# Performance work log

Hardware: AMD Instinct MI355X
Metric: run time of the kernel (lower is better)

The kernel has to match this reference:

```python
import jax, jax.numpy as jnp
import numpy as np

TAU = 1.0
K_TAU = 1.0
MAX_K = 64


def setup_inputs() -> dict:
    key = jax.random.key(0)
    ks = jax.random.split(key, 6)
    B, S, D, H = 8, 4096, 1024, 2048
    token_embeddings = jax.random.normal(ks[0], (B, S, D), dtype=jnp.float32)
    W1 = jax.random.normal(ks[1], (D, H), dtype=jnp.float32) * (1.0 / np.sqrt(D))
    b1 = jnp.zeros((H,), dtype=jnp.float32)
    W2 = jax.random.normal(ks[2], (H, 1), dtype=jnp.float32) * (1.0 / np.sqrt(H))
    b2 = jnp.zeros((1,), dtype=jnp.float32)
    k_logits = jax.random.normal(ks[3], (MAX_K,), dtype=jnp.float32) * 0.02
    return {"token_embeddings": token_embeddings, "W1": W1, "b1": b1,
            "W2": W2, "b2": b2, "k_logits": k_logits}


def _gumbel(rng, shape):
    u = jax.random.uniform(rng, shape, minval=1e-08, maxval=1.0 - 1e-08)
    return -jnp.log(-jnp.log(u))


def reference(token_embeddings, W1, b1, W2, b2, k_logits):
    B, S, D = token_embeddings.shape
    # scorer: Dense -> relu -> Dense(1), squeeze -> [B, S]
    h = jax.nn.relu(jnp.einsum('bsd,dh->bsh', token_embeddings, W1) + b1)
    importance_logits = (jnp.einsum('bsh,ho->bso', h, W2) + b2)[..., 0]

    rng = jax.random.key(42)  # training rng
    rng1, rng2 = jax.random.split(rng)

    # learnable-k selection (training branch)
    k_gumbel = _gumbel(rng1, k_logits.shape)
    k_soft = jax.nn.softmax((k_logits + k_gumbel) / K_TAU)
    expected_k = jnp.sum(k_soft * jnp.arange(1, MAX_K + 1, dtype=k_soft.dtype))
    k_selected = jnp.argmax(k_soft) + 1  # traced int scalar

    # gumbel-softmax hard top-k over tokens
    perturbed = importance_logits + _gumbel(rng2, importance_logits.shape)
    soft_mask = jax.nn.softmax(perturbed / TAU, axis=-1)  # [B, S]
    # rank of each token (0 = smallest); top-k == rank >= S - k
    rank = jnp.argsort(jnp.argsort(soft_mask, axis=-1), axis=-1)
    hard_mask = (rank >= S - k_selected).astype(soft_mask.dtype)
    selection_mask = jax.lax.stop_gradient(hard_mask - soft_mask) + soft_mask

    filtered_embeddings = token_embeddings * selection_mask[..., None]
    return filtered_embeddings, selection_mask, expected_k
```

## Files before the change

### kernel.cpp

```cpp
#include <hip/hip_runtime.h>
#include <stdint.h>

#define B_BATCH 8
#define S_SEQ   4096
#define D_DIM   1024
#define H_DIM   2048
#define M_TOK   (B_BATCH * S_SEQ)
#define MAXK    64
#define NSPLIT  2

typedef unsigned int u32;
typedef unsigned short u16;
typedef unsigned long long u64;
typedef __attribute__((ext_vector_type(8))) short short8;
typedef __attribute__((ext_vector_type(4))) float f32x4;

#define GLOBAL_AS __attribute__((address_space(1)))
#define LDS_AS    __attribute__((address_space(3)))


#define TF_ROUND(x0, x1, r) { x0 += x1; x1 = ((x1 << r) | (x1 >> (32 - r))); x1 ^= x0; }

__device__ __forceinline__ void tf2x32(u32 k0, u32 k1, u32 x0, u32 x1, u32& o0, u32& o1) {
  u32 k2 = k0 ^ k1 ^ 0x1BD11BDAu;
  x0 += k0; x1 += k1;
  TF_ROUND(x0, x1, 13) TF_ROUND(x0, x1, 15) TF_ROUND(x0, x1, 26) TF_ROUND(x0, x1, 6)
  x0 += k1; x1 += k2 + 1u;
  TF_ROUND(x0, x1, 17) TF_ROUND(x0, x1, 29) TF_ROUND(x0, x1, 16) TF_ROUND(x0, x1, 24)
  x0 += k2; x1 += k0 + 2u;
  TF_ROUND(x0, x1, 13) TF_ROUND(x0, x1, 15) TF_ROUND(x0, x1, 26) TF_ROUND(x0, x1, 6)
  x0 += k0; x1 += k1 + 3u;
  TF_ROUND(x0, x1, 17) TF_ROUND(x0, x1, 29) TF_ROUND(x0, x1, 16) TF_ROUND(x0, x1, 24)
  x0 += k1; x1 += k2 + 4u;
  TF_ROUND(x0, x1, 13) TF_ROUND(x0, x1, 15) TF_ROUND(x0, x1, 26) TF_ROUND(x0, x1, 6)
  x0 += k2; x1 += k0 + 5u;
  o0 = x0; o1 = x1;
}

__device__ __forceinline__ void jax_subkeys(u32& r1a, u32& r1b, u32& r2a, u32& r2b) {
  tf2x32(0u, 42u, 0u, 0u, r1a, r1b);
  tf2x32(0u, 42u, 0u, 1u, r2a, r2b);
}

__device__ __forceinline__ u32 jax_bits32(u32 ka, u32 kb, u32 i) {
  u32 o0, o1;
  tf2x32(ka, kb, 0u, i, o0, o1);
  return o0 ^ o1;
}

__device__ __forceinline__ float jax_uniform_from_bits(u32 bits) {
  float f = __uint_as_float((bits >> 9) | 0x3f800000u) - 1.0f;
  float r = f + 1e-8f;
  return fmaxf(1e-8f, r);
}

__device__ __forceinline__ float gumbel_from_bits(u32 bits) {
  float u = jax_uniform_from_bits(bits);
  return -logf(-logf(u));
}

__device__ __forceinline__ u32 ordf(float v) {
  u32 b = __float_as_uint(v);
  return (b & 0x80000000u) ? ~b : (b | 0x80000000u);
}

__device__ __forceinline__ u64 shflx64(u64 v, int m) {
  unsigned lo = (unsigned)v, hi = (unsigned)(v >> 32);
  lo = (unsigned)__shfl_xor((int)lo, m);
  hi = (unsigned)__shfl_xor((int)hi, m);
  return ((u64)hi << 32) | lo;
}


__device__ __forceinline__ u16 f2bf_rn(float x) {
  u32 u = __float_as_uint(x);
  u32 r = u + 0x7fffu + ((u >> 16) & 1u);
  return (u16)(r >> 16);
}

__device__ __forceinline__ void split1(float x, u16& h, u16& lo) {
  h = f2bf_rn(x);
  float hf = __uint_as_float(((u32)h) << 16);
  lo = f2bf_rn(x - hf);
}


__global__ __launch_bounds__(256) void split_a_kernel(const float* __restrict__ x,
                                                      u16* __restrict__ hi,
                                                      u16* __restrict__ lo) {
  const size_t i = ((size_t)blockIdx.x * 256 + threadIdx.x) * 4;
  float4 v = *(const float4*)(x + i);
  u16 h0, h1, h2, h3, l0, l1, l2, l3;
  split1(v.x, h0, l0); split1(v.y, h1, l1); split1(v.z, h2, l2); split1(v.w, h3, l3);
  u64 hv = (u64)h0 | ((u64)h1 << 16) | ((u64)h2 << 32) | ((u64)h3 << 48);
  u64 lv = (u64)l0 | ((u64)l1 << 16) | ((u64)l2 << 32) | ((u64)l3 << 48);
  *(u64*)(hi + i) = hv;
  *(u64*)(lo + i) = lv;
}

__global__ __launch_bounds__(256) void split_w1t_kernel(const float* __restrict__ W1,
                                                        u16* __restrict__ bhi,
                                                        u16* __restrict__ blo) {
  __shared__ float tile[32][33];
  const int tx = threadIdx.x & 31, ty = threadIdx.x >> 5;
  const int n0 = blockIdx.x * 32, k0 = blockIdx.y * 32;
  #pragma unroll
  for (int r = 0; r < 4; ++r)
    tile[ty + r * 8][tx] = W1[(size_t)(k0 + ty + r * 8) * H_DIM + n0 + tx];
  __syncthreads();
  #pragma unroll
  for (int r = 0; r < 4; ++r) {
    const int n = n0 + ty + r * 8, k = k0 + tx;
    u16 h, l;
    split1(tile[tx][ty + r * 8], h, l);
    bhi[(size_t)n * D_DIM + k] = h;
    blo[(size_t)n * D_DIM + k] = l;
  }
}


__device__ __forceinline__ void stage16(const u16* g, u16* l) {
  __builtin_amdgcn_global_load_lds((const GLOBAL_AS u32*)g, (LDS_AS u32*)l, 16, 0, 0);
}

__global__ __launch_bounds__(256, 2) void scorer_mfma(
    const u16* __restrict__ Ahi, const u16* __restrict__ Alo,
    const u16* __restrict__ Bhi, const u16* __restrict__ Blo,
    const float* __restrict__ b1, const float* __restrict__ W2,
    float* __restrict__ pl) {
  __shared__ u16 smem[4 * 128 * 32];
  u16* sAhi = smem;
  u16* sAlo = smem + 4096;
  u16* sBhi = smem + 8192;
  u16* sBlo = smem + 12288;

  const int tid = threadIdx.x;
  const int w = tid >> 6;
  const int l = tid & 63;
  const int m0 = blockIdx.x * 128;
  const int nyb = blockIdx.y;

  const int rl0 = w * 32 + (l >> 2);
  const int rl1 = rl0 + 16;
  const int kloc0 = (((l & 3) ^ ((rl0 >> 1) & 3)) << 3);
  const int kloc1 = (((l & 3) ^ ((rl1 >> 1) & 3)) << 3);
  const int lb0 = (w * 32) * 32;
  const int lb1 = (w * 32 + 16) * 32;

  int a_off[4], b_off[4];
  #pragma unroll
  for (int i = 0; i < 4; ++i) {
    int row = ((w & 1) << 6) + i * 16 + (l & 15);
    int slot = (l >> 4) ^ ((row >> 1) & 3);
    a_off[i] = row * 32 + slot * 8;
    int nrow = ((w >> 1) << 6) + i * 16 + (l & 15);
    int nslot = (l >> 4) ^ ((nrow >> 1) & 3);
    b_off[i] = nrow * 32 + nslot * 8;
  }

  float logit[4][4];
  #pragma unroll
  for (int i = 0; i < 4; ++i)
    #pragma unroll
    for (int r = 0; r < 4; ++r) logit[i][r] = 0.f;

  for (int t8 = 0; t8 < H_DIM / (128 * NSPLIT); ++t8) {
    const int n0 = nyb * (H_DIM / NSPLIT) + t8 * 128;
    f32x4 acc[4][4];
    #pragma unroll
    for (int i = 0; i < 4; ++i)
      #pragma unroll
      for (int j = 0; j < 4; ++j) acc[i][j] = (f32x4){0.f, 0.f, 0.f, 0.f};

    const u16* pA0h = Ahi + (size_t)(m0 + rl0) * D_DIM + kloc0;
    const u16* pA1h = Ahi + (size_t)(m0 + rl1) * D_DIM + kloc1;
    const u16* pA0l = Alo + (size_t)(m0 + rl0) * D_DIM + kloc0;
    const u16* pA1l = Alo + (size_t)(m0 + rl1) * D_DIM + kloc1;
    const u16* pB0h = Bhi + (size_t)(n0 + rl0) * D_DIM + kloc0;
    const u16* pB1h = Bhi + (size_t)(n0 + rl1) * D_DIM + kloc1;
    const u16* pB0l = Blo + (size_t)(n0 + rl0) * D_DIM + kloc0;
    const u16* pB1l = Blo + (size_t)(n0 + rl1) * D_DIM + kloc1;

    for (int k0 = 0; k0 < D_DIM; k0 += 32) {
      __syncthreads();
      stage16(pA0h, sAhi + lb0); stage16(pA1h, sAhi + lb1);
      stage16(pA0l, sAlo + lb0); stage16(pA1l, sAlo + lb1);
      stage16(pB0h, sBhi + lb0); stage16(pB1h, sBhi + lb1);
      stage16(pB0l, sBlo + lb0); stage16(pB1l, sBlo + lb1);
      pA0h += 32; pA1h += 32; pA0l += 32; pA1l += 32;
      pB0h += 32; pB1h += 32; pB0l += 32; pB1l += 32;
      __syncthreads();

      short8 ah[4], al[4], bh[4], bl[4];
      #pragma unroll
      for (int i = 0; i < 4; ++i) {
        ah[i] = *(const short8*)(sAhi + a_off[i]);
        al[i] = *(const short8*)(sAlo + a_off[i]);
        bh[i] = *(const short8*)(sBhi + b_off[i]);
        bl[i] = *(const short8*)(sBlo + b_off[i]);
      }
      #pragma unroll
      for (int i = 0; i < 4; ++i)
        #pragma unroll
        for (int j = 0; j < 4; ++j) {
          acc[i][j] = __builtin_amdgcn_mfma_f32_16x16x32_bf16(ah[i], bh[j], acc[i][j], 0, 0, 0);
          acc[i][j] = __builtin_amdgcn_mfma_f32_16x16x32_bf16(ah[i], bl[j], acc[i][j], 0, 0, 0);
          acc[i][j] = __builtin_amdgcn_mfma_f32_16x16x32_bf16(al[i], bh[j], acc[i][j], 0, 0, 0);
        }
    }

    const int nb = n0 + ((w >> 1) << 6);
    #pragma unroll
    for (int j = 0; j < 4; ++j) {
      const int n = nb + j * 16 + (l & 15);
      const float b1v = b1[n];
      const float w2v = W2[n];
      #pragma unroll
      for (int i = 0; i < 4; ++i)
        #pragma unroll
        for (int r = 0; r < 4; ++r)
          logit[i][r] += fmaxf(acc[i][j][r] + b1v, 0.f) * w2v;
    }
  }

  __syncthreads();
  float* red = (float*)smem;
  const int col = (l & 15) + ((w >> 1) << 4);
  #pragma unroll
  for (int i = 0; i < 4; ++i)
    #pragma unroll
    for (int r = 0; r < 4; ++r) {
      const int m = ((w & 1) << 6) + i * 16 + ((l >> 4) << 2) + r;
      red[m * 33 + col] = logit[i][r];
    }
  __syncthreads();
  if (tid < 128) {
    float s = 0.f;
    #pragma unroll
    for (int x = 0; x < 32; ++x) s += red[tid * 33 + x];
    pl[(size_t)nyb * M_TOK + m0 + tid] = s;
  }
}


__global__ __launch_bounds__(256) void scorer_kernel(
    const float* __restrict__ emb, const float* __restrict__ W1,
    const float* __restrict__ b1, const float* __restrict__ W2,
    const float* __restrict__ b2, float* __restrict__ pert) {
  __shared__ float As[16][68];
  __shared__ float Bs[16][132];
  __shared__ float red[64][17];

  const int tid = threadIdx.x;
  const int tx = tid & 15;
  const int ty = tid >> 4;
  const int m0 = blockIdx.x * 64;
  const int at = tid >> 2;
  const int ac = (tid & 3) << 2;
  const int br = tid >> 4;
  const int bc = (tid & 15) << 3;

  float logit[4] = {0.f, 0.f, 0.f, 0.f};

  for (int n0 = 0; n0 < H_DIM; n0 += 128) {
    float acc[4][8];
    #pragma unroll
    for (int i = 0; i < 4; i++)
      #pragma unroll
      for (int j = 0; j < 8; j++) acc[i][j] = 0.f;

    for (int k0 = 0; k0 < D_DIM; k0 += 16) {
      float4 av  = *(const float4*)(emb + (size_t)(m0 + at) * D_DIM + (k0 + ac));
      float4 bv0 = *(const float4*)(W1 + (size_t)(k0 + br) * H_DIM + (n0 + bc));
      float4 bv1 = *(const float4*)(W1 + (size_t)(k0 + br) * H_DIM + (n0 + bc) + 4);
      __syncthreads();
      As[ac + 0][at] = av.x; As[ac + 1][at] = av.y;
      As[ac + 2][at] = av.z; As[ac + 3][at] = av.w;
      *(float4*)&Bs[br][bc]     = bv0;
      *(float4*)&Bs[br][bc + 4] = bv1;
      __syncthreads();
      #pragma unroll
      for (int k = 0; k < 16; k++) {
        float4 a   = *(const float4*)&As[k][ty << 2];
        float4 b0  = *(const float4*)&Bs[k][tx << 3];
        float4 b1v = *(const float4*)&Bs[k][(tx << 3) + 4];
        float aa[4] = {a.x, a.y, a.z, a.w};
        float bb[8] = {b0.x, b0.y, b0.z, b0.w, b1v.x, b1v.y, b1v.z, b1v.w};
        #pragma unroll
        for (int i = 0; i < 4; i++)
          #pragma unroll
          for (int j = 0; j < 8; j++)
            acc[i][j] = fmaf(aa[i], bb[j], acc[i][j]);
      }
    }
    float4 c0 = *(const float4*)(b1 + n0 + (tx << 3));
    float4 c1 = *(const float4*)(b1 + n0 + (tx << 3) + 4);
    float4 w0 = *(const float4*)(W2 + n0 + (tx << 3));
    float4 w1 = *(const float4*)(W2 + n0 + (tx << 3) + 4);
    float cb[8] = {c0.x, c0.y, c0.z, c0.w, c1.x, c1.y, c1.z, c1.w};
    float wb[8] = {w0.x, w0.y, w0.z, w0.w, w1.x, w1.y, w1.z, w1.w};
    #pragma unroll
    for (int i = 0; i < 4; i++)
      #pragma unroll
      for (int j = 0; j < 8; j++) {
        float h = fmaxf(acc[i][j] + cb[j], 0.f);
        logit[i] = fmaf(h, wb[j], logit[i]);
      }
  }

  __syncthreads();
  #pragma unroll
  for (int i = 0; i < 4; i++) red[(ty << 2) + i][tx] = logit[i];
  __syncthreads();

  if (tid < 64) {
    float s = 0.f;
    #pragma unroll
    for (int x = 0; x < 16; x++) s += red[tid][x];
    s += b2[0];
    int t = m0 + tid;
    u32 r1a, r1b, r2a, r2b;
    jax_subkeys(r1a, r1b, r2a, r2b);
    pert[t] = s + gumbel_from_bits(jax_bits32(r2a, r2b, (u32)t));
  }
}


template <bool FROM_PL>
__device__ __forceinline__ void topk_body(const float* kl, const float* pl,
                                          const float* b2, float* mask,
                                          float* expk) {
  const int r = blockIdx.x;
  const int tid = threadIdx.x;
  const int w = tid >> 6, l = tid & 63;
  __shared__ int ksel_sh;
  __shared__ int cnt[2][4];

  u32 r1a, r1b, r2a, r2b;
  jax_subkeys(r1a, r1b, r2a, r2b);

  if (tid < 64) {
    float p = kl[l] + gumbel_from_bits(jax_bits32(r1a, r1b, (u32)l));
    u64 kkey = ((u64)ordf(p) << 32) | (unsigned)(63 - l);
    #pragma unroll
    for (int off = 32; off >= 1; off >>= 1) {
      u64 o = shflx64(kkey, off);
      if (o > kkey) kkey = o;
    }
    if (l == 0) ksel_sh = 64 - (int)(kkey & 0xffffffffu);
    if (r == 0) {
      float m = p;
      #pragma unroll
      for (int off = 32; off >= 1; off >>= 1) m = fmaxf(m, __shfl_xor(m, off));
      float e = expf(p - m);
      float s = e;
      #pragma unroll
      for (int off = 32; off >= 1; off >>= 1) s += __shfl_xor(s, off);
      float v = (e / s) * (float)(l + 1);
      #pragma unroll
      for (int off = 32; off >= 1; off >>= 1) v += __shfl_xor(v, off);
      if (l == 0) expk[0] = v;
    }
  }
  __syncthreads();
  const int k = ksel_sh;
  const float b2v = FROM_PL ? b2[0] : 0.f;

  u64 keys[16];
  #pragma unroll
  for (int j = 0; j < 16; j++) {
    int s = tid + (j << 8);
    int t = (r << 12) + s;
    float v;
    if (FROM_PL) {
      float acc = pl[t];
      #pragma unroll
      for (int q = 1; q < NSPLIT; ++q) acc += pl[(size_t)q * M_TOK + t];
      v = acc + b2v + gumbel_from_bits(jax_bits32(r2a, r2b, (u32)t));
    } else {
      v = mask[t];
    }
    keys[j] = ((u64)ordf(v) << 12) | (unsigned)s;
  }

  u64 lo = 0ull, hi = (1ull << 44) - 1ull;
  int it = 0;
  while (lo < hi) {
    const u64 mid = (lo + hi + 1ull) >> 1;
    int c = 0;
    #pragma unroll
    for (int j = 0; j < 16; j++) c += (keys[j] >= mid) ? 1 : 0;
    #pragma unroll
    for (int off = 32; off >= 1; off >>= 1) c += __shfl_xor(c, off);
    const int buf = it & 1;
    if (l == 0) cnt[buf][w] = c;
    __syncthreads();
    const int tot = cnt[buf][0] + cnt[buf][1] + cnt[buf][2] + cnt[buf][3];
    if (tot >= k) lo = mid; else hi = mid - 1ull;
    ++it;
  }
  const u64 thresh = lo;

  #pragma unroll
  for (int j = 0; j < 16; j++) {
    int s = tid + (j << 8);
    mask[(r << 12) + s] = (keys[j] >= thresh) ? 1.0f : 0.0f;
  }
}

__global__ __launch_bounds__(256) void topk_pl_kernel(const float* __restrict__ kl,
                                                      const float* __restrict__ pl,
                                                      const float* __restrict__ b2,
                                                      float* __restrict__ mask,
                                                      float* __restrict__ expk) {
  topk_body<true>(kl, pl, b2, mask, expk);
}

__global__ __launch_bounds__(256) void topk_kernel(const float* __restrict__ kl,
                                                   float* __restrict__ mask,
                                                   float* __restrict__ expk) {
  topk_body<false>(kl, nullptr, nullptr, mask, expk);
}


__global__ __launch_bounds__(256) void filter_kernel(const float* __restrict__ emb,
                                                     const float* __restrict__ mask,
                                                     float* __restrict__ out) {
  const int t = blockIdx.x;
  const float mk = mask[t];
  const size_t base = (size_t)t * D_DIM + ((size_t)threadIdx.x << 2);
  float4 v = *(const float4*)(emb + base);
  *(float4*)(out + base) = make_float4(v.x * mk, v.y * mk, v.z * mk, v.w * mk);
}


extern "C" void kernel_launch(void* const* d_in, const int* in_sizes, int n_in,
                              void* d_out, int out_size, void* d_ws, size_t ws_size,
                              hipStream_t stream) {
  const float* emb = (const float*)d_in[0];
  const float* W1  = (const float*)d_in[1];
  const float* b1  = (const float*)d_in[2];
  const float* W2  = (const float*)d_in[3];
  const float* b2  = (const float*)d_in[4];
  const float* kl  = (const float*)d_in[5];
  float* out  = (float*)d_out;
  float* mask = out + (size_t)M_TOK * D_DIM;
  float* expk = mask + M_TOK;

  const size_t ws_need = (size_t)H_DIM * D_DIM * 2 * 2 + (size_t)NSPLIT * M_TOK * 4;

  if (ws_size >= ws_need) {
    u16* Ahi = (u16*)d_out;
    u16* Alo = Ahi + (size_t)M_TOK * D_DIM;
    u16* Bhi = (u16*)d_ws;
    u16* Blo = Bhi + (size_t)H_DIM * D_DIM;
    float* pl = (float*)(Blo + (size_t)H_DIM * D_DIM);

    split_a_kernel<<<M_TOK * D_DIM / 1024, 256, 0, stream>>>(emb, Ahi, Alo);
    split_w1t_kernel<<<dim3(H_DIM / 32, D_DIM / 32), 256, 0, stream>>>(W1, Bhi, Blo);
    scorer_mfma<<<dim3(M_TOK / 128, NSPLIT), 256, 0, stream>>>(Ahi, Alo, Bhi, Blo, b1, W2, pl);
    topk_pl_kernel<<<B_BATCH, 256, 0, stream>>>(kl, pl, b2, mask, expk);
  } else {
    scorer_kernel<<<M_TOK / 64, 256, 0, stream>>>(emb, W1, b1, W2, b2, mask);
    topk_kernel<<<B_BATCH, 256, 0, stream>>>(kl, mask, expk);
  }

  filter_kernel<<<M_TOK, 256, 0, stream>>>(emb, mask, out);
}
```

Measured before the change: 707.5 us.

## Fuse split kernels, remap scorer blocks across XCDs, grid-stride filter

```diff
diff --git a/kernel.cpp b/kernel.cpp
--- a/kernel.cpp
+++ b/kernel.cpp
@@ -85,36 +85,40 @@
 }
 
 
-__global__ __launch_bounds__(256) void split_a_kernel(const float* __restrict__ x,
-                                                      u16* __restrict__ hi,
-                                                      u16* __restrict__ lo) {
-  const size_t i = ((size_t)blockIdx.x * 256 + threadIdx.x) * 4;
-  float4 v = *(const float4*)(x + i);
-  u16 h0, h1, h2, h3, l0, l1, l2, l3;
-  split1(v.x, h0, l0); split1(v.y, h1, l1); split1(v.z, h2, l2); split1(v.w, h3, l3);
-  u64 hv = (u64)h0 | ((u64)h1 << 16) | ((u64)h2 << 32) | ((u64)h3 << 48);
-  u64 lv = (u64)l0 | ((u64)l1 << 16) | ((u64)l2 << 32) | ((u64)l3 << 48);
-  *(u64*)(hi + i) = hv;
-  *(u64*)(lo + i) = lv;
-}
-
-__global__ __launch_bounds__(256) void split_w1t_kernel(const float* __restrict__ W1,
-                                                        u16* __restrict__ bhi,
-                                                        u16* __restrict__ blo) {
-  __shared__ float tile[32][33];
-  const int tx = threadIdx.x & 31, ty = threadIdx.x >> 5;
-  const int n0 = blockIdx.x * 32, k0 = blockIdx.y * 32;
-  #pragma unroll
-  for (int r = 0; r < 4; ++r)
-    tile[ty + r * 8][tx] = W1[(size_t)(k0 + ty + r * 8) * H_DIM + n0 + tx];
-  __syncthreads();
-  #pragma unroll
-  for (int r = 0; r < 4; ++r) {
-    const int n = n0 + ty + r * 8, k = k0 + tx;
-    u16 h, l;
-    split1(tile[tx][ty + r * 8], h, l);
-    bhi[(size_t)n * D_DIM + k] = h;
-    blo[(size_t)n * D_DIM + k] = l;
+#define NA_BLK 4096
+
+__global__ __launch_bounds__(256) void split_fuse(
+    const float* __restrict__ emb, u16* __restrict__ Ahi, u16* __restrict__ Alo,
+    const float* __restrict__ W1, u16* __restrict__ Bhi, u16* __restrict__ Blo) {
+  if (blockIdx.x < NA_BLK) {
+    const size_t total = (size_t)M_TOK * D_DIM / 4;
+    for (size_t g = (size_t)blockIdx.x * 256 + threadIdx.x; g < total;
+         g += (size_t)NA_BLK * 256) {
+      float4 v = ((const float4*)emb)[g];
+      u16 h0, h1, h2, h3, l0, l1, l2, l3;
+      split1(v.x, h0, l0); split1(v.y, h1, l1); split1(v.z, h2, l2); split1(v.w, h3, l3);
+      u64 hv = (u64)h0 | ((u64)h1 << 16) | ((u64)h2 << 32) | ((u64)h3 << 48);
+      u64 lv = (u64)l0 | ((u64)l1 << 16) | ((u64)l2 << 32) | ((u64)l3 << 48);
+      ((u64*)Ahi)[g] = hv;
+      ((u64*)Alo)[g] = lv;
+    }
+  } else {
+    __shared__ float tile[32][33];
+    const int wb = blockIdx.x - NA_BLK;
+    const int n0 = (wb & 63) * 32, k0 = (wb >> 6) * 32;
+    const int tx = threadIdx.x & 31, ty = threadIdx.x >> 5;
+    #pragma unroll
+    for (int r = 0; r < 4; ++r)
+      tile[ty + r * 8][tx] = W1[(size_t)(k0 + ty + r * 8) * H_DIM + n0 + tx];
+    __syncthreads();
+    #pragma unroll
+    for (int r = 0; r < 4; ++r) {
+      const int n = n0 + ty + r * 8, k = k0 + tx;
+      u16 h, l;
+      split1(tile[tx][ty + r * 8], h, l);
+      Bhi[(size_t)n * D_DIM + k] = h;
+      Blo[(size_t)n * D_DIM + k] = l;
+    }
   }
 }
 
@@ -137,8 +141,11 @@
   const int tid = threadIdx.x;
   const int w = tid >> 6;
   const int l = tid & 63;
-  const int m0 = blockIdx.x * 128;
-  const int nyb = blockIdx.y;
+
+  const int b = blockIdx.x;
+  const int xcd = b & 7;
+  const int nyb = xcd & 1;
+  const int m0 = ((b >> 3) * 4 + (xcd >> 1)) * 128;
 
   const int rl0 = w * 32 + (l >> 2);
   const int rl1 = rl0 + 16;
@@ -426,11 +433,13 @@
 __global__ __launch_bounds__(256) void filter_kernel(const float* __restrict__ emb,
                                                      const float* __restrict__ mask,
                                                      float* __restrict__ out) {
-  const int t = blockIdx.x;
-  const float mk = mask[t];
-  const size_t base = (size_t)t * D_DIM + ((size_t)threadIdx.x << 2);
-  float4 v = *(const float4*)(emb + base);
-  *(float4*)(out + base) = make_float4(v.x * mk, v.y * mk, v.z * mk, v.w * mk);
+  const size_t total = (size_t)M_TOK * D_DIM / 4;
+  for (size_t g = (size_t)blockIdx.x * 256 + threadIdx.x; g < total;
+       g += (size_t)gridDim.x * 256) {
+    const float mk = mask[g >> 8];
+    float4 v = ((const float4*)emb)[g];
+    ((float4*)out)[g] = make_float4(v.x * mk, v.y * mk, v.z * mk, v.w * mk);
+  }
 }
 
 
@@ -456,14 +465,13 @@
     u16* Blo = Bhi + (size_t)H_DIM * D_DIM;
     float* pl = (float*)(Blo + (size_t)H_DIM * D_DIM);
 
-    split_a_kernel<<<M_TOK * D_DIM / 1024, 256, 0, stream>>>(emb, Ahi, Alo);
-    split_w1t_kernel<<<dim3(H_DIM / 32, D_DIM / 32), 256, 0, stream>>>(W1, Bhi, Blo);
-    scorer_mfma<<<dim3(M_TOK / 128, NSPLIT), 256, 0, stream>>>(Ahi, Alo, Bhi, Blo, b1, W2, pl);
+    split_fuse<<<NA_BLK + 2048, 256, 0, stream>>>(emb, Ahi, Alo, W1, Bhi, Blo);
+    scorer_mfma<<<M_TOK / 128 * NSPLIT, 256, 0, stream>>>(Ahi, Alo, Bhi, Blo, b1, W2, pl);
     topk_pl_kernel<<<B_BATCH, 256, 0, stream>>>(kl, pl, b2, mask, expk);
   } else {
     scorer_kernel<<<M_TOK / 64, 256, 0, stream>>>(emb, W1, b1, W2, b2, mask);
     topk_kernel<<<B_BATCH, 256, 0, stream>>>(kl, mask, expk);
   }
 
-  filter_kernel<<<M_TOK, 256, 0, stream>>>(emb, mask, out);
-}
+  filter_kernel<<<2048, 256, 0, stream>>>(emb, mask, out);
+}
```

After: 712.2 us. About the same (+0.7%).
